# Optimization experiments

Measured on AMD Instinct MI355X. Metric: run time of the kernel, lower is better.

## Reference

```python
import jax, jax.numpy as jnp
import numpy as np

N = 50000
E = 1600000
IN, OUT = 128, 64


def _gcn(h, W, b, src, dst):
    # DGL GraphConv, norm='both', weight applied first (in>out), activation=relu
    x = h @ W  # [N, OUT]
    ones = jnp.ones((src.shape[0],), dtype=h.dtype)
    deg_out = jnp.clip(jax.ops.segment_sum(ones, src, num_segments=N), 1.0)
    deg_in = jnp.clip(jax.ops.segment_sum(ones, dst, num_segments=N), 1.0)
    x = x * jax.lax.rsqrt(deg_out)[:, None]
    agg = jax.ops.segment_sum(x[src], dst, num_segments=N)  # SpMM
    agg = agg * jax.lax.rsqrt(deg_in)[:, None]
    return jax.nn.relu(agg + b)


def setup_inputs() -> dict:
    key = jax.random.key(0)
    ks = jax.random.split(key, 10)
    inp = {"h": jax.random.normal(ks[0], (N, IN), dtype=jnp.float32)}
    for i in range(3):
        inp[f"src{i}"] = jax.random.randint(ks[1 + 2 * i], (E,), 0, N, dtype=jnp.int32)
        inp[f"dst{i}"] = jax.random.randint(ks[2 + 2 * i], (E,), 0, N, dtype=jnp.int32)
        inp[f"W{i}"] = jax.random.normal(ks[7 + i], (IN, OUT), dtype=jnp.float32) * (1.0 / np.sqrt(IN))
        inp[f"b{i}"] = jnp.zeros((OUT,), dtype=jnp.float32)
    return inp


def reference(h, src0, dst0, src1, dst1, src2, dst2, W0, b0, W1, b1, W2, b2):
    e0 = _gcn(h, W0, b0, src0, dst0)
    e1 = _gcn(h, W1, b1, src1, dst1)
    e2 = _gcn(h, W2, b2, src2, dst2)
    # stack over meta-path dim then mean == average of semantic embeddings
    return (e0 + e1 + e2) / 3.0
```

## Files before the change

### kernel.cpp

```cpp
#include <hip/hip_runtime.h>

#define KDIM 128
#define NCOLS 64
#define NHCH 64
#define HW 12500
#define BUCKET 64
#define NB7 782
#define FCAP 2816
#define NPB 85
#define PREP_HIST (3 * NHCH)
#define PREP_CNT  (3 * NPB)
#define PREP_WF   12
#define PREP_GRID (PREP_HIST + PREP_CNT + PREP_WF)
#define PG_PART (3 * NPB)
#define PG_GEMM_PER 391
#define PG_GEMM (3 * PG_GEMM_PER)
#define PG_GRID (PG_PART + PG_GEMM)

typedef __attribute__((ext_vector_type(8))) short bf16x8;
typedef __attribute__((ext_vector_type(4))) float f32x4;

struct GArgs {
  const int*   src[3];
  const int*   dst[3];
  const float* W[3];
  const float* b[3];
  int          E[3];
};

__device__ __forceinline__ unsigned short f2bf(float f) {
  unsigned u = __float_as_uint(f);
  u += 0x7FFFu + ((u >> 16) & 1u);
  return (unsigned short)(u >> 16);
}
__device__ __forceinline__ float bflo(unsigned u) { return __uint_as_float(u << 16); }
__device__ __forceinline__ float bfhi(unsigned u) { return __uint_as_float(u & 0xFFFF0000u); }

__device__ __forceinline__ bf16x8 ld_cvt8(const float* __restrict__ p) {
  float4 f0 = *(const float4*)p;
  float4 f1 = *(const float4*)(p + 4);
  union { uint4 u; bf16x8 v; } cv;
  cv.u.x = (unsigned)f2bf(f0.x) | ((unsigned)f2bf(f0.y) << 16);
  cv.u.y = (unsigned)f2bf(f0.z) | ((unsigned)f2bf(f0.w) << 16);
  cv.u.z = (unsigned)f2bf(f1.x) | ((unsigned)f2bf(f1.y) << 16);
  cv.u.w = (unsigned)f2bf(f1.z) | ((unsigned)f2bf(f1.w) << 16);
  return cv.v;
}

__global__ __launch_bounds__(256) void prep_kernel(
    GArgs A, unsigned short* __restrict__ Wf, unsigned* __restrict__ P8,
    int* __restrict__ tot, int* __restrict__ Pcnt) {
  __shared__ unsigned sbuf[HW];
  const int b = blockIdx.x;
  const int t = threadIdx.x;

  if (b < PREP_HIST) {
    const int g = b >> 6;
    const int chunk = b & 63;
    const int E = A.E[g];
    const int per_chunk = (((E + NHCH - 1) / NHCH) + 3) & ~3;
    const int* __restrict__ keys = A.src[g];
    for (int i = t; i < HW; i += 256) sbuf[i] = 0;
    __syncthreads();
    const int e0 = chunk * per_chunk;
    const int e1 = min(e0 + per_chunk, E);
    const int nn = max(e1 - e0, 0);
    const int nv = nn >> 2;
    const int4* k4p = (const int4*)&keys[e0];
    for (int v = t; v < nv; v += 256) {
      int4 k = k4p[v];
      atomicAdd(&sbuf[(unsigned)k.x >> 2], 1u << (((unsigned)k.x & 3u) * 8));
      atomicAdd(&sbuf[(unsigned)k.y >> 2], 1u << (((unsigned)k.y & 3u) * 8));
      atomicAdd(&sbuf[(unsigned)k.z >> 2], 1u << (((unsigned)k.z & 3u) * 8));
      atomicAdd(&sbuf[(unsigned)k.w >> 2], 1u << (((unsigned)k.w & 3u) * 8));
    }
    for (int e = e0 + (nv << 2) + t; e < e1; e += 256) {
      unsigned k = (unsigned)keys[e];
      atomicAdd(&sbuf[k >> 2], 1u << ((k & 3u) * 8));
    }
    __syncthreads();
    unsigned* __restrict__ dstp = P8 + (size_t)b * HW;
    for (int i = t; i < HW; i += 256) dstp[i] = sbuf[i];

  } else if (b < PREP_HIST + PREP_CNT) {
    const int bb = b - PREP_HIST;
    const int g = bb / NPB;
    const int blk = bb % NPB;
    const int E = A.E[g];
    const int per_block = (((E + NPB - 1) / NPB) + 3) & ~3;
    const int* __restrict__ dst = A.dst[g];
    int* hcnt = (int*)sbuf;
    for (int i = t; i < NB7; i += 256) hcnt[i] = 0;
    __syncthreads();
    const int e0 = blk * per_block;
    const int e1 = min(e0 + per_block, E);
    const int nn = max(e1 - e0, 0);
    const int nv = nn >> 2;
    const int4* d4 = (const int4*)&dst[e0];
    for (int v = t; v < nv; v += 256) {
      int4 d = d4[v];
      atomicAdd(&hcnt[(unsigned)d.x >> 6], 1);
      atomicAdd(&hcnt[(unsigned)d.y >> 6], 1);
      atomicAdd(&hcnt[(unsigned)d.z >> 6], 1);
      atomicAdd(&hcnt[(unsigned)d.w >> 6], 1);
    }
    for (int e = e0 + (nv << 2) + t; e < e1; e += 256)
      atomicAdd(&hcnt[(unsigned)dst[e] >> 6], 1);
    __syncthreads();
    int* __restrict__ pc = Pcnt + (size_t)bb * NB7;
    for (int i = t; i < NB7; i += 256) {
      int c = hcnt[i];
      pc[i] = c;
      if (c) atomicAdd(&tot[g * NB7 + i], c);
    }

  } else {
    int tid = (b - PREP_HIST - PREP_CNT) * 256 + t;
    int lane = tid & 63;
    int frag = (tid >> 6) & 15;
    int g = tid >> 10;
    int c = frag >> 2, kk = frag & 3;
    int n = lane & 15, quad = lane >> 4;
    const float* W = A.W[g];
    unsigned short v[8];
    #pragma unroll
    for (int j = 0; j < 8; ++j) {
      int k = 32 * kk + quad * 8 + j;
      v[j] = f2bf(W[k * 64 + 4 * n + c]);
    }
    uint4 u;
    u.x = (unsigned)v[0] | ((unsigned)v[1] << 16);
    u.y = (unsigned)v[2] | ((unsigned)v[3] << 16);
    u.z = (unsigned)v[4] | ((unsigned)v[5] << 16);
    u.w = (unsigned)v[6] | ((unsigned)v[7] << 16);
    ((uint4*)Wf)[tid] = u;
  }
}

__global__ __launch_bounds__(512) void pg_kernel(
    GArgs A, const float* __restrict__ h,
    const unsigned short* __restrict__ Wf, const unsigned* __restrict__ P8,
    const int* __restrict__ tot, const int* __restrict__ Pcnt,
    int* __restrict__ cursor, int* __restrict__ off, unsigned* __restrict__ P2,
    unsigned short* __restrict__ x, int N, int Emax) {
  __shared__ int lcnt[NB7];
  __shared__ int lcur[NB7];
  __shared__ int sd[512];
  const int b = blockIdx.x;
  const int t = threadIdx.x;

  if (b < PG_PART) {
    const int g = b / NPB;
    const int blk = b % NPB;
    const int E = A.E[g];
    const int per_block = (((E + NPB - 1) / NPB) + 3) & ~3;
    const int* __restrict__ src = A.src[g];
    const int* __restrict__ dst = A.dst[g];
    unsigned* __restrict__ P2g = P2 + (size_t)g * Emax;

    const int* __restrict__ pc = Pcnt + (size_t)b * NB7;
    for (int i = t; i < NB7; i += 512) lcnt[i] = pc[i];

    int base = 0;
    for (int c0 = 0; c0 < NB7; c0 += 512) {
      int idx = c0 + t;
      int v = (idx < NB7) ? tot[g * NB7 + idx] : 0;
      sd[t] = v;
      __syncthreads();
      for (int o = 1; o < 512; o <<= 1) {
        int add = (t >= o) ? sd[t - o] : 0;
        __syncthreads();
        sd[t] += add;
        __syncthreads();
      }
      int excl = base + sd[t] - v;
      if (idx < NB7) {
        lcur[idx] = excl;
        if (blk == 0) off[g * (NB7 + 1) + idx] = excl;
      }
      base += sd[511];
      __syncthreads();
    }
    if (blk == 0 && t == 0) off[g * (NB7 + 1) + NB7] = base;

    for (int i = t; i < NB7; i += 512) {
      int c = lcnt[i];
      if (c) lcur[i] += atomicAdd(&cursor[g * NB7 + i], c);
    }
    __syncthreads();

    const int e0 = blk * per_block;
    const int e1 = min(e0 + per_block, E);
    const int nn = max(e1 - e0, 0);
    const int nv = nn >> 2;
    const int4* d4 = (const int4*)&dst[e0];
    const int4* s4 = (const int4*)&src[e0];
    for (int v = t; v < nv; v += 512) {
      int4 d = d4[v];
      int4 s = s4[v];
      unsigned bk; int pos;
      bk = (unsigned)d.x >> 6; pos = atomicAdd(&lcur[bk], 1);
      P2g[pos] = (unsigned)s.x | (((unsigned)d.x & 63u) << 16);
      bk = (unsigned)d.y >> 6; pos = atomicAdd(&lcur[bk], 1);
      P2g[pos] = (unsigned)s.y | (((unsigned)d.y & 63u) << 16);
      bk = (unsigned)d.z >> 6; pos = atomicAdd(&lcur[bk], 1);
      P2g[pos] = (unsigned)s.z | (((unsigned)d.z & 63u) << 16);
      bk = (unsigned)d.w >> 6; pos = atomicAdd(&lcur[bk], 1);
      P2g[pos] = (unsigned)s.w | (((unsigned)d.w & 63u) << 16);
    }
    for (int e = e0 + (nv << 2) + t; e < e1; e += 512) {
      unsigned d = (unsigned)dst[e];
      unsigned bk = d >> 6;
      int pos = atomicAdd(&lcur[bk], 1);
      P2g[pos] = (unsigned)src[e] | ((d & 63u) << 16);
    }

  } else {
    unsigned* ldegw = (unsigned*)lcnt;
    const int gb = b - PG_PART;
    const int g = gb / PG_GEMM_PER;
    const int blk = gb % PG_GEMM_PER;
    const int row0 = blk * 128;
    unsigned short* __restrict__ xg = x + (size_t)g * N * NCOLS;

    if (t < 64) ldegw[t] = 0;
    __syncthreads();
    if (t < 256) {
      const unsigned* __restrict__ Pg = P8 + (size_t)g * NHCH * HW;
      const int widx = t >> 3;
      const int cg = t & 7;
      const int wcol = min((row0 >> 2) + widx, HW - 1);
      unsigned lo = 0, hi = 0;
      #pragma unroll
      for (int cc = 0; cc < 8; ++cc) {
        unsigned wv = Pg[(size_t)(cg * 8 + cc) * HW + wcol];
        lo += wv & 0x00FF00FFu;
        hi += (wv >> 8) & 0x00FF00FFu;
      }
      atomicAdd(&ldegw[2 * widx], lo);
      atomicAdd(&ldegw[2 * widx + 1], hi);
    }

    const int lane = t & 63;
    const int w = t >> 6;
    const int quad = lane >> 4;
    const int n = lane & 15;

    int arow = min(row0 + w * 16 + n, N - 1);
    const float* hrowf = h + (size_t)arow * KDIM + quad * 8;
    bf16x8 a0 = ld_cvt8(hrowf);
    bf16x8 a1 = ld_cvt8(hrowf + 32);
    bf16x8 a2 = ld_cvt8(hrowf + 64);
    bf16x8 a3 = ld_cvt8(hrowf + 96);

    const uint4* wfp = (const uint4*)Wf + (size_t)g * 1024 + lane;

    f32x4 acc[4];
    #pragma unroll
    for (int c = 0; c < 4; ++c) acc[c] = (f32x4)(0.f);

    __syncthreads();

    #pragma unroll
    for (int c = 0; c < 4; ++c) {
      union { uint4 u; bf16x8 v; } b0, b1, b2, b3;
      b0.u = wfp[(size_t)(c * 4 + 0) * 64];
      b1.u = wfp[(size_t)(c * 4 + 1) * 64];
      b2.u = wfp[(size_t)(c * 4 + 2) * 64];
      b3.u = wfp[(size_t)(c * 4 + 3) * 64];
      acc[c] = __builtin_amdgcn_mfma_f32_16x16x32_bf16(a0, b0.v, acc[c], 0, 0, 0);
      acc[c] = __builtin_amdgcn_mfma_f32_16x16x32_bf16(a1, b1.v, acc[c], 0, 0, 0);
      acc[c] = __builtin_amdgcn_mfma_f32_16x16x32_bf16(a2, b2.v, acc[c], 0, 0, 0);
      acc[c] = __builtin_amdgcn_mfma_f32_16x16x32_bf16(a3, b3.v, acc[c], 0, 0, 0);
    }

    const int rbase = row0 + w * 16 + quad * 4;
    #pragma unroll
    for (int r = 0; r < 4; ++r) {
      int row = rbase + r;
      if (row < N) {
        int lr = row - row0;
        float dg = (float)((ldegw[2 * (lr >> 2) + (lr & 1)] >> (((lr >> 1) & 1) * 16)) & 0xFFFFu);
        float s = rsqrtf(fmaxf(dg, 1.0f));
        uint2 o;
        o.x = (unsigned)f2bf(acc[0][r] * s) | ((unsigned)f2bf(acc[1][r] * s) << 16);
        o.y = (unsigned)f2bf(acc[2][r] * s) | ((unsigned)f2bf(acc[3][r] * s) << 16);
        *(uint2*)(xg + (size_t)row * NCOLS + 4 * n) = o;
      }
    }
  }
}

__global__ __launch_bounds__(512) void spmm_all_kernel(
    GArgs A, const unsigned* __restrict__ P2, const int* __restrict__ off,
    const unsigned short* __restrict__ x, float* __restrict__ out,
    int N, int Emax) {
  __shared__ unsigned eb[FCAP];
  __shared__ unsigned short srcs[FCAP];
  __shared__ int cnt[BUCKET];
  __shared__ int cur[BUCKET];
  __shared__ int rsx[BUCKET + 1];

  const int t = threadIdx.x;
  const int bk = blockIdx.x;
  const int dbase = bk * BUCKET;
  const int nd = min(BUCKET, N - dbase);
  const int grp = t >> 3;
  const int qe = (t & 7) * 8;

  float tot[8];
  #pragma unroll
  for (int j = 0; j < 8; ++j) tot[j] = 0.f;

  for (int g = 0; g < 3; ++g) {
    const unsigned* __restrict__ P2g = P2 + (size_t)g * Emax;
    const unsigned short* __restrict__ xg = x + (size_t)g * N * NCOLS;

    __syncthreads();
    if (t < BUCKET) cnt[t] = 0;
    __syncthreads();

    const int e0 = off[g * (NB7 + 1) + bk];
    const int ne = min(off[g * (NB7 + 1) + bk + 1] - e0, FCAP);
    for (int i = t; i < ne; i += 512) {
      unsigned e = P2g[e0 + i];
      eb[i] = e;
      atomicAdd(&cnt[e >> 16], 1);
    }
    __syncthreads();

    if (t < BUCKET) {
      int v = cnt[t];
      int incl = v;
      #pragma unroll
      for (int o = 1; o < 64; o <<= 1) {
        int u = __shfl_up(incl, o, 64);
        if (t >= o) incl += u;
      }
      rsx[t + 1] = incl;
      cur[t] = incl - v;
      if (t == 0) rsx[0] = 0;
    }
    __syncthreads();

    for (int i = t; i < ne; i += 512) {
      unsigned e = eb[i];
      int pos = atomicAdd(&cur[e >> 16], 1);
      srcs[pos] = (unsigned short)(e & 0xFFFFu);
    }
    __syncthreads();

    if (grp < nd) {
      int i = rsx[grp];
      const int iend = rsx[grp + 1];
      const int deg = iend - i;
      float acc[8];
      #pragma unroll
      for (int j = 0; j < 8; ++j) acc[j] = 0.f;
      for (; i + 3 < iend; i += 4) {
        int sa = srcs[i + 0];
        int sb = srcs[i + 1];
        int sc = srcs[i + 2];
        int sdd = srcs[i + 3];
        uint4 ua = *(const uint4*)&xg[(size_t)sa * NCOLS + qe];
        uint4 ub = *(const uint4*)&xg[(size_t)sb * NCOLS + qe];
        uint4 uc = *(const uint4*)&xg[(size_t)sc * NCOLS + qe];
        uint4 ud = *(const uint4*)&xg[(size_t)sdd * NCOLS + qe];
        acc[0] += bflo(ua.x) + bflo(ub.x) + bflo(uc.x) + bflo(ud.x);
        acc[1] += bfhi(ua.x) + bfhi(ub.x) + bfhi(uc.x) + bfhi(ud.x);
        acc[2] += bflo(ua.y) + bflo(ub.y) + bflo(uc.y) + bflo(ud.y);
        acc[3] += bfhi(ua.y) + bfhi(ub.y) + bfhi(uc.y) + bfhi(ud.y);
        acc[4] += bflo(ua.z) + bflo(ub.z) + bflo(uc.z) + bflo(ud.z);
        acc[5] += bfhi(ua.z) + bfhi(ub.z) + bfhi(uc.z) + bfhi(ud.z);
        acc[6] += bflo(ua.w) + bflo(ub.w) + bflo(uc.w) + bflo(ud.w);
        acc[7] += bfhi(ua.w) + bfhi(ub.w) + bfhi(uc.w) + bfhi(ud.w);
      }
      for (; i < iend; ++i) {
        int s = srcs[i];
        uint4 u = *(const uint4*)&xg[(size_t)s * NCOLS + qe];
        acc[0] += bflo(u.x); acc[1] += bfhi(u.x);
        acc[2] += bflo(u.y); acc[3] += bfhi(u.y);
        acc[4] += bflo(u.z); acc[5] += bfhi(u.z);
        acc[6] += bflo(u.w); acc[7] += bfhi(u.w);
      }
      float sc2 = rsqrtf(fmaxf((float)deg, 1.0f));
      const float* bg = A.b[g] + qe;
      #pragma unroll
      for (int j = 0; j < 8; ++j)
        tot[j] += fmaxf(fmaf(acc[j], sc2, bg[j]), 0.f) * (1.0f / 3.0f);
    }
  }

  if (grp < nd) {
    float* op = &out[(size_t)(dbase + grp) * NCOLS + qe];
    *(float4*)&op[0] = make_float4(tot[0], tot[1], tot[2], tot[3]);
    *(float4*)&op[4] = make_float4(tot[4], tot[5], tot[6], tot[7]);
  }
}

extern "C" void kernel_launch(void* const* d_in, const int* in_sizes, int n_in,
                              void* d_out, int out_size, void* d_ws, size_t ws_size,
                              hipStream_t stream) {
  const float* h = (const float*)d_in[0];
  const int N = in_sizes[0] / KDIM;
  float* out = (float*)d_out;

  GArgs A;
  int Emax = 0;
  for (int g = 0; g < 3; ++g) {
    A.src[g] = (const int*)  d_in[1 + g * 4];
    A.dst[g] = (const int*)  d_in[2 + g * 4];
    A.W[g]   = (const float*)d_in[3 + g * 4];
    A.b[g]   = (const float*)d_in[4 + g * 4];
    A.E[g]   = in_sizes[1 + g * 4];
    if (A.E[g] > Emax) Emax = A.E[g];
  }

  char* w = (char*)d_ws;
  unsigned short* x = (unsigned short*)w;
  char* w2 = w + (size_t)3 * N * NCOLS * sizeof(unsigned short);
  unsigned* P2 = (unsigned*)w2;
  char* w3 = w2 + (size_t)3 * Emax * sizeof(unsigned);
  unsigned* P8 = (unsigned*)w3;
  char* w4 = w3 + (size_t)3 * NHCH * HW * sizeof(unsigned);
  unsigned short* Wf = (unsigned short*)w4;
  char* w5 = w4 + (size_t)3 * 16 * 64 * 8 * sizeof(unsigned short);
  int* Pcnt = (int*)w5;
  char* w6 = w5 + (size_t)3 * NPB * NB7 * sizeof(int);
  int* tot    = (int*)w6;
  int* cursor = tot + 3 * NB7;
  int* off    = cursor + 3 * NB7;

  hipMemsetAsync(tot, 0, 2 * 3 * NB7 * sizeof(int), stream);
  prep_kernel<<<PREP_GRID, 256, 0, stream>>>(A, Wf, P8, tot, Pcnt);
  pg_kernel<<<PG_GRID, 512, 0, stream>>>(A, h, Wf, P8, tot, Pcnt, cursor, off, P2, x, N, Emax);
  spmm_all_kernel<<<NB7, 512, 0, stream>>>(A, P2, off, x, out, N, Emax);
}
```

Measured before the change: 257.6 us.

## Halve SpMM bucket size and split each destination row across two thread groups

Destination buckets shrink from 64 to 32 nodes, doubling the number of SpMM blocks and the histogram/partition bin counts. Each destination row is now handled by two 8-lane groups that take alternating edges, and their partial sums are combined with a cross-lane shuffle. The aim is more parallelism and more memory-level parallelism in the gather-bound SpMM, at the cost of larger prefix scans and more per-block atomics and overhead in the partition stages. The smaller per-bucket edge capacity (1408) leaves less headroom if a bucket receives more edges than expected.

```diff
diff --git a/kernel.cpp b/kernel.cpp
--- a/kernel.cpp
+++ b/kernel.cpp
@@ -4,9 +4,9 @@
 #define NCOLS 64
 #define NHCH 64
 #define HW 12500
-#define BUCKET 64
-#define NB7 782
-#define FCAP 2816
+#define BUCKET 32
+#define NB5 1563
+#define FCAP 1408
 #define NPB 85
 #define PREP_HIST (3 * NHCH)
 #define PREP_CNT  (3 * NPB)
@@ -90,7 +90,7 @@
     const int per_block = (((E + NPB - 1) / NPB) + 3) & ~3;
     const int* __restrict__ dst = A.dst[g];
     int* hcnt = (int*)sbuf;
-    for (int i = t; i < NB7; i += 256) hcnt[i] = 0;
+    for (int i = t; i < NB5; i += 256) hcnt[i] = 0;
     __syncthreads();
     const int e0 = blk * per_block;
     const int e1 = min(e0 + per_block, E);
@@ -99,19 +99,19 @@
     const int4* d4 = (const int4*)&dst[e0];
     for (int v = t; v < nv; v += 256) {
       int4 d = d4[v];
-      atomicAdd(&hcnt[(unsigned)d.x >> 6], 1);
-      atomicAdd(&hcnt[(unsigned)d.y >> 6], 1);
-      atomicAdd(&hcnt[(unsigned)d.z >> 6], 1);
-      atomicAdd(&hcnt[(unsigned)d.w >> 6], 1);
+      atomicAdd(&hcnt[(unsigned)d.x >> 5], 1);
+      atomicAdd(&hcnt[(unsigned)d.y >> 5], 1);
+      atomicAdd(&hcnt[(unsigned)d.z >> 5], 1);
+      atomicAdd(&hcnt[(unsigned)d.w >> 5], 1);
     }
     for (int e = e0 + (nv << 2) + t; e < e1; e += 256)
-      atomicAdd(&hcnt[(unsigned)dst[e] >> 6], 1);
-    __syncthreads();
-    int* __restrict__ pc = Pcnt + (size_t)bb * NB7;
-    for (int i = t; i < NB7; i += 256) {
+      atomicAdd(&hcnt[(unsigned)dst[e] >> 5], 1);
+    __syncthreads();
+    int* __restrict__ pc = Pcnt + (size_t)bb * NB5;
+    for (int i = t; i < NB5; i += 256) {
       int c = hcnt[i];
       pc[i] = c;
-      if (c) atomicAdd(&tot[g * NB7 + i], c);
+      if (c) atomicAdd(&tot[g * NB5 + i], c);
     }
 
   } else {
@@ -143,8 +143,8 @@
     const int* __restrict__ tot, const int* __restrict__ Pcnt,
     int* __restrict__ cursor, int* __restrict__ off, unsigned* __restrict__ P2,
     unsigned short* __restrict__ x, int N, int Emax) {
-  __shared__ int lcnt[NB7];
-  __shared__ int lcur[NB7];
+  __shared__ int lcnt[NB5];
+  __shared__ int lcur[NB5];
   __shared__ int sd[512];
   const int b = blockIdx.x;
   const int t = threadIdx.x;
@@ -158,13 +158,13 @@
     const int* __restrict__ dst = A.dst[g];
     unsigned* __restrict__ P2g = P2 + (size_t)g * Emax;
 
-    const int* __restrict__ pc = Pcnt + (size_t)b * NB7;
-    for (int i = t; i < NB7; i += 512) lcnt[i] = pc[i];
+    const int* __restrict__ pc = Pcnt + (size_t)b * NB5;
+    for (int i = t; i < NB5; i += 512) lcnt[i] = pc[i];
 
     int base = 0;
-    for (int c0 = 0; c0 < NB7; c0 += 512) {
+    for (int c0 = 0; c0 < NB5; c0 += 512) {
       int idx = c0 + t;
-      int v = (idx < NB7) ? tot[g * NB7 + idx] : 0;
+      int v = (idx < NB5) ? tot[g * NB5 + idx] : 0;
       sd[t] = v;
       __syncthreads();
       for (int o = 1; o < 512; o <<= 1) {
@@ -174,18 +174,18 @@
         __syncthreads();
       }
       int excl = base + sd[t] - v;
-      if (idx < NB7) {
+      if (idx < NB5) {
         lcur[idx] = excl;
-        if (blk == 0) off[g * (NB7 + 1) + idx] = excl;
+        if (blk == 0) off[g * (NB5 + 1) + idx] = excl;
       }
       base += sd[511];
       __syncthreads();
     }
-    if (blk == 0 && t == 0) off[g * (NB7 + 1) + NB7] = base;
-
-    for (int i = t; i < NB7; i += 512) {
+    if (blk == 0 && t == 0) off[g * (NB5 + 1) + NB5] = base;
+
+    for (int i = t; i < NB5; i += 512) {
       int c = lcnt[i];
-      if (c) lcur[i] += atomicAdd(&cursor[g * NB7 + i], c);
+      if (c) lcur[i] += atomicAdd(&cursor[g * NB5 + i], c);
     }
     __syncthreads();
 
@@ -199,20 +199,20 @@
       int4 d = d4[v];
       int4 s = s4[v];
       unsigned bk; int pos;
-      bk = (unsigned)d.x >> 6; pos = atomicAdd(&lcur[bk], 1);
-      P2g[pos] = (unsigned)s.x | (((unsigned)d.x & 63u) << 16);
-      bk = (unsigned)d.y >> 6; pos = atomicAdd(&lcur[bk], 1);
-      P2g[pos] = (unsigned)s.y | (((unsigned)d.y & 63u) << 16);
-      bk = (unsigned)d.z >> 6; pos = atomicAdd(&lcur[bk], 1);
-      P2g[pos] = (unsigned)s.z | (((unsigned)d.z & 63u) << 16);
-      bk = (unsigned)d.w >> 6; pos = atomicAdd(&lcur[bk], 1);
-      P2g[pos] = (unsigned)s.w | (((unsigned)d.w & 63u) << 16);
+      bk = (unsigned)d.x >> 5; pos = atomicAdd(&lcur[bk], 1);
+      P2g[pos] = (unsigned)s.x | (((unsigned)d.x & 31u) << 16);
+      bk = (unsigned)d.y >> 5; pos = atomicAdd(&lcur[bk], 1);
+      P2g[pos] = (unsigned)s.y | (((unsigned)d.y & 31u) << 16);
+      bk = (unsigned)d.z >> 5; pos = atomicAdd(&lcur[bk], 1);
+      P2g[pos] = (unsigned)s.z | (((unsigned)d.z & 31u) << 16);
+      bk = (unsigned)d.w >> 5; pos = atomicAdd(&lcur[bk], 1);
+      P2g[pos] = (unsigned)s.w | (((unsigned)d.w & 31u) << 16);
     }
     for (int e = e0 + (nv << 2) + t; e < e1; e += 512) {
       unsigned d = (unsigned)dst[e];
-      unsigned bk = d >> 6;
+      unsigned bk = d >> 5;
       int pos = atomicAdd(&lcur[bk], 1);
-      P2g[pos] = (unsigned)src[e] | ((d & 63u) << 16);
+      P2g[pos] = (unsigned)src[e] | ((d & 31u) << 16);
     }
 
   } else {
@@ -306,6 +306,8 @@
   const int dbase = bk * BUCKET;
   const int nd = min(BUCKET, N - dbase);
   const int grp = t >> 3;
+  const int ni = grp >> 1;
+  const int half = grp & 1;
   const int qe = (t & 7) * 8;
 
   float tot[8];
@@ -320,8 +322,8 @@
     if (t < BUCKET) cnt[t] = 0;
     __syncthreads();
 
-    const int e0 = off[g * (NB7 + 1) + bk];
-    const int ne = min(off[g * (NB7 + 1) + bk + 1] - e0, FCAP);
+    const int e0 = off[g * (NB5 + 1) + bk];
+    const int ne = min(off[g * (NB5 + 1) + bk + 1] - e0, FCAP);
     for (int i = t; i < ne; i += 512) {
       unsigned e = P2g[e0 + i];
       eb[i] = e;
@@ -333,7 +335,7 @@
       int v = cnt[t];
       int incl = v;
       #pragma unroll
-      for (int o = 1; o < 64; o <<= 1) {
+      for (int o = 1; o < BUCKET; o <<= 1) {
         int u = __shfl_up(incl, o, 64);
         if (t >= o) incl += u;
       }
@@ -350,18 +352,19 @@
     }
     __syncthreads();
 
-    if (grp < nd) {
-      int i = rsx[grp];
-      const int iend = rsx[grp + 1];
-      const int deg = iend - i;
+    if (ni < nd) {
+      const int ibase = rsx[ni];
+      const int iend = rsx[ni + 1];
+      const int deg = iend - ibase;
       float acc[8];
       #pragma unroll
       for (int j = 0; j < 8; ++j) acc[j] = 0.f;
-      for (; i + 3 < iend; i += 4) {
+      int i = ibase + half;
+      for (; i + 6 < iend; i += 8) {
         int sa = srcs[i + 0];
-        int sb = srcs[i + 1];
-        int sc = srcs[i + 2];
-        int sdd = srcs[i + 3];
+        int sb = srcs[i + 2];
+        int sc = srcs[i + 4];
+        int sdd = srcs[i + 6];
         uint4 ua = *(const uint4*)&xg[(size_t)sa * NCOLS + qe];
         uint4 ub = *(const uint4*)&xg[(size_t)sb * NCOLS + qe];
         uint4 uc = *(const uint4*)&xg[(size_t)sc * NCOLS + qe];
@@ -375,7 +378,7 @@
         acc[6] += bflo(ua.w) + bflo(ub.w) + bflo(uc.w) + bflo(ud.w);
         acc[7] += bfhi(ua.w) + bfhi(ub.w) + bfhi(uc.w) + bfhi(ud.w);
       }
-      for (; i < iend; ++i) {
+      for (; i < iend; i += 2) {
         int s = srcs[i];
         uint4 u = *(const uint4*)&xg[(size_t)s * NCOLS + qe];
         acc[0] += bflo(u.x); acc[1] += bfhi(u.x);
@@ -383,6 +386,8 @@
         acc[4] += bflo(u.z); acc[5] += bfhi(u.z);
         acc[6] += bflo(u.w); acc[7] += bfhi(u.w);
       }
+      #pragma unroll
+      for (int j = 0; j < 8; ++j) acc[j] += __shfl_xor(acc[j], 8, 64);
       float sc2 = rsqrtf(fmaxf((float)deg, 1.0f));
       const float* bg = A.b[g] + qe;
       #pragma unroll
@@ -391,8 +396,8 @@
     }
   }
 
-  if (grp < nd) {
-    float* op = &out[(size_t)(dbase + grp) * NCOLS + qe];
+  if (ni < nd && half == 0) {
+    float* op = &out[(size_t)(dbase + ni) * NCOLS + qe];
     *(float4*)&op[0] = make_float4(tot[0], tot[1], tot[2], tot[3]);
     *(float4*)&op[4] = make_float4(tot[4], tot[5], tot[6], tot[7]);
   }
@@ -426,13 +431,13 @@
   unsigned short* Wf = (unsigned short*)w4;
   char* w5 = w4 + (size_t)3 * 16 * 64 * 8 * sizeof(unsigned short);
   int* Pcnt = (int*)w5;
-  char* w6 = w5 + (size_t)3 * NPB * NB7 * sizeof(int);
+  char* w6 = w5 + (size_t)3 * NPB * NB5 * sizeof(int);
   int* tot    = (int*)w6;
-  int* cursor = tot + 3 * NB7;
-  int* off    = cursor + 3 * NB7;
-
-  hipMemsetAsync(tot, 0, 2 * 3 * NB7 * sizeof(int), stream);
+  int* cursor = tot + 3 * NB5;
+  int* off    = cursor + 3 * NB5;
+
+  hipMemsetAsync(tot, 0, 2 * 3 * NB5 * sizeof(int), stream);
   prep_kernel<<<PREP_GRID, 256, 0, stream>>>(A, Wf, P8, tot, Pcnt);
   pg_kernel<<<PG_GRID, 512, 0, stream>>>(A, h, Wf, P8, tot, Pcnt, cursor, off, P2, x, N, Emax);
-  spmm_all_kernel<<<NB7, 512, 0, stream>>>(A, P2, off, x, out, N, Emax);
-}
+  spmm_all_kernel<<<NB5, 512, 0, stream>>>(A, P2, off, x, out, N, Emax);
+}
```

Result: slower. 266.4 us (+3.4%).
